# Kernel optimization log

Hardware: AMD Instinct MI355X
Metric: run time of the kernel (lower is better)

## Reference

```python
import jax, jax.numpy as jnp
import numpy as np

H = 256
N0, N1, N2 = 150000, 80000, 20000
E0, E1 = 800000, 300000


def setup_inputs() -> dict:
    key = jax.random.key(0)
    ks = jax.random.split(key, 16)
    sc = 1.0 / np.sqrt(H)
    return {
        "x": jax.random.normal(ks[0], (N0, H), jnp.float32),
        # GATConv params (heads=1): lin weight, att_src, att_dst, bias
        "W_gat": jax.random.normal(ks[1], (H, H), jnp.float32) * sc,
        "att_src": jax.random.normal(ks[2], (H,), jnp.float32) * sc,
        "att_dst": jax.random.normal(ks[3], (H,), jnp.float32) * sc,
        "b_gat": jax.random.normal(ks[4], (H,), jnp.float32) * 0.01,
        # SAGEConv layer 0: lin_l (aggregated, with bias), lin_r (root, no bias)
        "Wl0": jax.random.normal(ks[5], (H, H), jnp.float32) * sc,
        "bl0": jnp.zeros((H,), jnp.float32),
        "Wr0": jax.random.normal(ks[6], (H, H), jnp.float32) * sc,
        # SAGEConv layer 1
        "Wl1": jax.random.normal(ks[7], (H, H), jnp.float32) * sc,
        "bl1": jnp.zeros((H,), jnp.float32),
        "Wr1": jax.random.normal(ks[8], (H, H), jnp.float32) * sc,
        # NeighborSampler bipartite edge lists (src -> dst)
        "src0": jax.random.randint(ks[9], (E0,), 0, N0, dtype=jnp.int32),
        "dst0": jax.random.randint(ks[10], (E0,), 0, N1, dtype=jnp.int32),
        "src1": jax.random.randint(ks[11], (E1,), 0, N1, dtype=jnp.int32),
        "dst1": jax.random.randint(ks[12], (E1,), 0, N2, dtype=jnp.int32),
        "n1": N1,
        "n2": N2,
    }


def _gat(x, src, dst, W, a_s, a_d, b):
    """PyG GATConv, heads=1, add_self_loops=True, eval mode (dropout no-op)."""
    N = x.shape[0]
    h = x @ W                                   # [N, H]
    loops = jnp.arange(N, dtype=src.dtype)      # self loops over all N nodes
    s = jnp.concatenate([src, loops])
    d = jnp.concatenate([dst, loops])
    al_s = (h * a_s).sum(-1)                    # [N]
    al_d = (h * a_d).sum(-1)                    # [N]
    e = jax.nn.leaky_relu(al_s[s] + al_d[d], 0.2)
    m = jax.ops.segment_max(e, d, num_segments=N)     # softmax over dst groups
    w = jnp.exp(e - m[d])
    z = jax.ops.segment_sum(w, d, num_segments=N)
    coef = w / z[d]
    out = jax.ops.segment_sum(coef[:, None] * h[s], d, num_segments=N)
    return out + b


def _sage(x_src, x_tgt, src, dst, n_tgt, Wl, bl, Wr):
    """PyG SAGEConv((x, x_target), edge_index), mean aggr, normalize=True."""
    msg = x_src[src]                                         # [E, H]
    ssum = jax.ops.segment_sum(msg, dst, num_segments=n_tgt)
    cnt = jax.ops.segment_sum(jnp.ones(src.shape, msg.dtype), dst,
                              num_segments=n_tgt)
    mean = ssum / jnp.maximum(cnt, 1.0)[:, None]
    out = mean @ Wl + bl + x_tgt @ Wr
    nrm = jnp.linalg.norm(out, axis=-1, keepdims=True)       # F.normalize
    return out / jnp.maximum(nrm, 1e-12)


def reference(x, W_gat, att_src, att_dst, b_gat, Wl0, bl0, Wr0, Wl1, bl1, Wr1,
              src0, dst0, src1, dst1, n1, n2):
    # Layer 0 (its result is discarded by the original module: x = x_all each
    # iteration and only the final x is appended to xs).
    h0 = _gat(x, src0, dst0, W_gat, att_src, att_dst, b_gat)
    _ = jax.nn.relu(_sage(h0, h0[:n1], src0, dst0, n1, Wl0, bl0, Wr0))
    # Layer 1 (the returned output)
    h1 = _gat(x, src1, dst1, W_gat, att_src, att_dst, b_gat)
    out = _sage(h1, h1[:n2], src1, dst1, n2, Wl1, bl1, Wr1)
    return out
```

## Files before the change

kernel.cpp:

```cpp
#include <hip/hip_runtime.h>


#define NS 80000
#define ND 20000

typedef float   float4v  __attribute__((ext_vector_type(4)));
typedef float   f32x4    __attribute__((ext_vector_type(4)));
typedef __bf16  bf16x8   __attribute__((ext_vector_type(8)));
typedef unsigned short ushort8v __attribute__((ext_vector_type(8)));
typedef unsigned short ushort2v __attribute__((ext_vector_type(2)));
typedef int     int4v    __attribute__((ext_vector_type(4)));

union frag_u { ushort8v u; bf16x8 b; };

__device__ __forceinline__ float us2f(unsigned short u) {
    union { unsigned int i; float f; } x; x.i = ((unsigned)u) << 16; return x.f;
}
__device__ __forceinline__ unsigned short f2us(float f) {
    union { __bf16 b; unsigned short u; } x; x.b = (__bf16)f; return x.u;
}
__device__ __forceinline__ float lrelu02(float x) { return x > 0.f ? x : 0.2f * x; }

__global__ __launch_bounds__(256) void prep_misc(
    const float* __restrict__ Wg, const float* __restrict__ Wl,
    const float* __restrict__ Wr, unsigned short* __restrict__ Wgt,
    unsigned short* __restrict__ Wcat, int* __restrict__ zerop, int nz4)
{
    const int b = blockIdx.x, t = threadIdx.x;
    if (b < 256) {
        Wgt[b * 256 + t] = f2us(Wg[t * 256 + b]);
    } else if (b < 512) {
        const int n = b - 256;
        Wcat[n * 512 + t]       = f2us(Wl[t * 256 + n]);
        Wcat[n * 512 + 256 + t] = f2us(Wr[t * 256 + n]);
    } else {
        const int i = (b - 512) * 256 + t;
        if (i < nz4) ((int4v*)zerop)[i] = (int4v){0, 0, 0, 0};
    }
}

template <int EPI, bool AF32, bool COUNT>
__global__ __launch_bounds__(512) void gemm_mfma(
    const void* __restrict__ Av, const unsigned short* __restrict__ Bt,
    int M, int K,
    unsigned short* __restrict__ hb_out,
    const float* __restrict__ avs, const float* __restrict__ avd,
    float* __restrict__ al_s, float* __restrict__ al_d,
    const float* __restrict__ bias, float* __restrict__ outp,
    int nblk, const int* __restrict__ dstE, int* __restrict__ cnt,
    int* __restrict__ rank, int E)
{
    __shared__ __align__(16) unsigned short Als[2][128][40];
    __shared__ __align__(16) unsigned short Bls[2][256][40];
    __shared__ float red0[128];
    __shared__ float red1[128];

    if (COUNT && (int)blockIdx.x >= nblk) {
        const int i = ((int)blockIdx.x - nblk) * 512 + (int)threadIdx.x;
        if (i < E) rank[i] = atomicAdd(&cnt[dstE[i]], 1);
        return;
    }

    const int tid  = threadIdx.x;
    const int lane = tid & 63;
    const int wid  = tid >> 6;
    const int wr   = wid >> 2;
    const int wc   = wid & 3;
    const int row0 = blockIdx.x * 128;
    const int lg   = lane >> 4;
    const int lm   = lane & 15;

    f32x4 acc[4][4] = {};

    const int arow = tid >> 2;
    const int akof = (tid & 3) * 8;
    const int brow = tid >> 1;
    const int bkof = (tid & 1) * 16;
    const int nk   = K >> 5;

    ushort8v avr, bvr0, bvr1;

    auto load_t = [&](int kt) {
        const int k0 = kt * 32;
        if constexpr (AF32) {
            const float* ag = (const float*)Av + (size_t)(row0 + arow) * K + k0 + akof;
            const float4v v0 = *(const float4v*)ag;
            const float4v v1 = *(const float4v*)(ag + 4);
            avr[0]=f2us(v0[0]); avr[1]=f2us(v0[1]); avr[2]=f2us(v0[2]); avr[3]=f2us(v0[3]);
            avr[4]=f2us(v1[0]); avr[5]=f2us(v1[1]); avr[6]=f2us(v1[2]); avr[7]=f2us(v1[3]);
        } else {
            if (row0 + arow < M) {
                avr = *(const ushort8v*)((const unsigned short*)Av + (size_t)(row0 + arow) * K + k0 + akof);
            } else {
                avr = (ushort8v){0,0,0,0,0,0,0,0};
            }
        }
        const unsigned short* bgp = Bt + (size_t)brow * K + k0 + bkof;
        bvr0 = *(const ushort8v*)bgp;
        bvr1 = *(const ushort8v*)(bgp + 8);
    };
    auto store_t = [&](int b) {
        *(ushort8v*)&Als[b][arow][akof]     = avr;
        *(ushort8v*)&Bls[b][brow][bkof]     = bvr0;
        *(ushort8v*)&Bls[b][brow][bkof + 8] = bvr1;
    };

    load_t(0); store_t(0); __syncthreads();
    if (nk > 1) load_t(1);
    int cur = 0;

    for (int kt = 0; kt < nk; ++kt) {
        frag_u af[4], bf[4];
#pragma unroll
        for (int m = 0; m < 4; ++m)
            af[m].u = *(const ushort8v*)&Als[cur][wr*64 + m*16 + lm][lg*8];
#pragma unroll
        for (int n = 0; n < 4; ++n)
            bf[n].u = *(const ushort8v*)&Bls[cur][wc*64 + n*16 + lm][lg*8];
#pragma unroll
        for (int m = 0; m < 4; ++m)
#pragma unroll
            for (int n = 0; n < 4; ++n)
                acc[m][n] = __builtin_amdgcn_mfma_f32_16x16x32_bf16(
                    af[m].b, bf[n].b, acc[m][n], 0, 0, 0);
        if (kt + 1 < nk) {
            store_t(cur ^ 1);
            __syncthreads();
            if (kt + 2 < nk) load_t(kt + 2);
            cur ^= 1;
        }
    }

    if constexpr (EPI == 0) {
        if (tid < 128) { red0[tid] = 0.f; red1[tid] = 0.f; }
        __syncthreads();
        float asv[4], adv[4], bgv[4];
#pragma unroll
        for (int n = 0; n < 4; ++n) {
            const int col = wc*64 + n*16 + lm;
            asv[n] = avs[col]; adv[n] = avd[col]; bgv[n] = bias[col];
        }
#pragma unroll
        for (int m = 0; m < 4; ++m) {
#pragma unroll
            for (int j = 0; j < 4; ++j) {
                const int lr = wr*64 + m*16 + lg*4 + j;
                float ps = 0.f, pd = 0.f;
#pragma unroll
                for (int n = 0; n < 4; ++n) {
                    const float v = acc[m][n][j];
                    ps += v * asv[n]; pd += v * adv[n];
                    hb_out[(size_t)(row0 + lr) * 256 + wc*64 + n*16 + lm] = f2us(v + bgv[n]);
                }
#pragma unroll
                for (int off = 1; off < 16; off <<= 1) {
                    ps += __shfl_xor(ps, off);
                    pd += __shfl_xor(pd, off);
                }
                if (lm == 0) { atomicAdd(&red0[lr], ps); atomicAdd(&red1[lr], pd); }
            }
        }
        __syncthreads();
        if (tid < 128) { al_s[row0 + tid] = red0[tid]; al_d[row0 + tid] = red1[tid]; }
    } else {
        if (tid < 128) red0[tid] = 0.f;
        __syncthreads();
        float bv[4];
#pragma unroll
        for (int n = 0; n < 4; ++n) bv[n] = bias[wc*64 + n*16 + lm];
#pragma unroll
        for (int m = 0; m < 4; ++m) {
#pragma unroll
            for (int j = 0; j < 4; ++j) {
                const int lr = wr*64 + m*16 + lg*4 + j;
                float ss = 0.f;
#pragma unroll
                for (int n = 0; n < 4; ++n) {
                    const float v = acc[m][n][j] + bv[n];
                    acc[m][n][j] = v;
                    ss += v * v;
                }
#pragma unroll
                for (int off = 1; off < 16; off <<= 1) ss += __shfl_xor(ss, off);
                if (lm == 0) atomicAdd(&red0[lr], ss);
            }
        }
        __syncthreads();
#pragma unroll
        for (int m = 0; m < 4; ++m) {
#pragma unroll
            for (int j = 0; j < 4; ++j) {
                const int lr = wr*64 + m*16 + lg*4 + j;
                const int grow = row0 + lr;
                if (grow < M) {
                    const float inv = 1.0f / fmaxf(sqrtf(red0[lr]), 1e-12f);
#pragma unroll
                    for (int n = 0; n < 4; ++n)
                        outp[(size_t)grow * 256 + wc*64 + n*16 + lm] = acc[m][n][j] * inv;
                }
            }
        }
    }
}

__global__ __launch_bounds__(1024) void scan_excl(
    const int* __restrict__ cnt, int* __restrict__ ptr, int n)
{
    __shared__ int part[1024];
    const int tid = threadIdx.x;
    const int chunk = (n + 1023) / 1024;
    const int i0 = tid * chunk;
    const int i1 = min(i0 + chunk, n);
    int s = 0;
    for (int i = i0; i < i1; ++i) s += cnt[i];
    part[tid] = s;
    __syncthreads();
    for (int off = 1; off < 1024; off <<= 1) {
        const int t = (tid >= off) ? part[tid - off] : 0;
        __syncthreads();
        part[tid] += t;
        __syncthreads();
    }
    int run = tid ? part[tid - 1] : 0;
    for (int i = i0; i < i1; ++i) { ptr[i] = run; run += cnt[i]; }
    if (tid == 1023) ptr[n] = part[1023];
}

__global__ void edge_scatter(const int* __restrict__ src, const int* __restrict__ dst,
                             const int* __restrict__ ptr, const int* __restrict__ rank,
                             const float* __restrict__ al_s, const float* __restrict__ al_d,
                             int* __restrict__ ssort, float* __restrict__ wbuf, int E)
{
    const int i = blockIdx.x * 256 + threadIdx.x;
    if (i < E) {
        const int d = dst[i];
        const int s = src[i];
        const int pos = ptr[d] + rank[i];
        ssort[pos] = s;
        wbuf[pos] = __expf(lrelu02(al_s[s] + al_d[d]));
    }
}

__global__ __launch_bounds__(128) void gat_sage(
    const unsigned short* __restrict__ hb, const float* __restrict__ al_s,
    const float* __restrict__ al_d, const int* __restrict__ ssort,
    const float* __restrict__ wbuf, const int* __restrict__ ptr,
    unsigned short* __restrict__ hcat)
{
    __shared__ float ldsg[4][264];
    __shared__ float ldss[4][264];
    __shared__ float zp[4];
    const int v    = blockIdx.x;
    const int tid  = threadIdx.x;
    const int slot = tid >> 5;
    const int l32  = tid & 31;
    const int c0   = l32 * 8;
    const int p0 = ptr[v], p1 = ptr[v + 1];

    const float w_self = __expf(lrelu02(al_s[v] + al_d[v]));

    float accg[8], accs[8];
    float zpart = 0.f;
#pragma unroll
    for (int j = 0; j < 8; ++j) accs[j] = 0.f;
    if (slot == 0) {
        const ushort8v hv = *(const ushort8v*)&hb[(size_t)v * 256 + c0];
#pragma unroll
        for (int j = 0; j < 8; ++j) accg[j] = w_self * us2f(hv[j]);
    } else {
#pragma unroll
        for (int j = 0; j < 8; ++j) accg[j] = 0.f;
    }

    int p = p0 + slot;
    for (; p + 4 < p1; p += 8) {
        const int s0 = ssort[p];
        const int s1 = ssort[p + 4];
        const float w0 = wbuf[p];
        const float w1 = wbuf[p + 4];
        const ushort8v h0 = *(const ushort8v*)&hb[(size_t)s0 * 256 + c0];
        const ushort8v h1 = *(const ushort8v*)&hb[(size_t)s1 * 256 + c0];
        zpart += w0 + w1;
        const bool g0 = (s0 >= ND), g1 = (s1 >= ND);
#pragma unroll
        for (int j = 0; j < 8; ++j) {
            const float f0 = us2f(h0[j]);
            const float f1 = us2f(h1[j]);
            accg[j] = fmaf(w0, f0, accg[j]);
            accg[j] = fmaf(w1, f1, accg[j]);
            accs[j] += (g0 ? f0 : 0.f) + (g1 ? f1 : 0.f);
        }
    }
    if (p < p1) {
        const int s0 = ssort[p];
        const float w0 = wbuf[p];
        const ushort8v h0 = *(const ushort8v*)&hb[(size_t)s0 * 256 + c0];
        zpart += w0;
        const bool g0 = (s0 >= ND);
#pragma unroll
        for (int j = 0; j < 8; ++j) {
            const float f0 = us2f(h0[j]);
            accg[j] = fmaf(w0, f0, accg[j]);
            accs[j] += g0 ? f0 : 0.f;
        }
    }

    if (l32 == 0) zp[slot] = zpart;
    *(f32x4*)&ldsg[slot][c0]     = (f32x4){accg[0], accg[1], accg[2], accg[3]};
    *(f32x4*)&ldsg[slot][c0 + 4] = (f32x4){accg[4], accg[5], accg[6], accg[7]};
    *(f32x4*)&ldss[slot][c0]     = (f32x4){accs[0], accs[1], accs[2], accs[3]};
    *(f32x4*)&ldss[slot][c0 + 4] = (f32x4){accs[4], accs[5], accs[6], accs[7]};
    __syncthreads();

    const float inv_z = 1.0f / (w_self + zp[0] + zp[1] + zp[2] + zp[3]);
    const int c = tid * 2;
    float rg0 = 0.f, rg1 = 0.f, rs0 = 0.f, rs1 = 0.f;
#pragma unroll
    for (int s2 = 0; s2 < 4; ++s2) {
        rg0 += ldsg[s2][c];     rg1 += ldsg[s2][c + 1];
        rs0 += ldss[s2][c];     rs1 += ldss[s2][c + 1];
    }
    *(ushort2v*)&hcat[(size_t)v * 512 + 256 + c] =
        (ushort2v){f2us(rg0 * inv_z), f2us(rg1 * inv_z)};
    *(ushort2v*)&hcat[(size_t)v * 512 + c] =
        (ushort2v){f2us(rs0), f2us(rs1)};
}

__global__ __launch_bounds__(256) void sage_fin(
    const int* __restrict__ ssort, const int* __restrict__ ptr,
    unsigned short* __restrict__ hcat)
{
    const int tid   = threadIdx.x;
    const int g     = tid >> 6;
    const int v     = blockIdx.x * 4 + g;
    const int slot2 = (tid >> 5) & 1;
    const int l32   = tid & 31;
    const int c0    = l32 * 8;
    const int p0 = ptr[v], p1 = ptr[v + 1];

    float acc[8];
    if (slot2 == 0) {
        const ushort8v pv = *(const ushort8v*)&hcat[(size_t)v * 512 + c0];
#pragma unroll
        for (int j = 0; j < 8; ++j) acc[j] = us2f(pv[j]);
    } else {
#pragma unroll
        for (int j = 0; j < 8; ++j) acc[j] = 0.f;
    }
    int p = p0 + slot2;
    for (; p + 2 < p1; p += 4) {
        const int s0 = ssort[p];
        const int s1 = ssort[p + 2];
        if (s0 < ND) {
            const ushort8v hv = *(const ushort8v*)&hcat[(size_t)s0 * 512 + 256 + c0];
#pragma unroll
            for (int j = 0; j < 8; ++j) acc[j] += us2f(hv[j]);
        }
        if (s1 < ND) {
            const ushort8v hv = *(const ushort8v*)&hcat[(size_t)s1 * 512 + 256 + c0];
#pragma unroll
            for (int j = 0; j < 8; ++j) acc[j] += us2f(hv[j]);
        }
    }
    if (p < p1) {
        const int s0 = ssort[p];
        if (s0 < ND) {
            const ushort8v hv = *(const ushort8v*)&hcat[(size_t)s0 * 512 + 256 + c0];
#pragma unroll
            for (int j = 0; j < 8; ++j) acc[j] += us2f(hv[j]);
        }
    }
#pragma unroll
    for (int j = 0; j < 8; ++j) acc[j] += __shfl_xor(acc[j], 32);

    const int deg = p1 - p0;
    const float inv = (deg > 0) ? 1.0f / (float)deg : 0.f;
    if (slot2 == 0) {
        ushort8v o;
#pragma unroll
        for (int j = 0; j < 8; ++j) o[j] = f2us(acc[j] * inv);
        *(ushort8v*)&hcat[(size_t)v * 512 + c0] = o;
    }
}

extern "C" void kernel_launch(void* const* d_in, const int* in_sizes, int n_in,
                              void* d_out, int out_size, void* d_ws, size_t ws_size,
                              hipStream_t stream)
{
    const float* x    = (const float*)d_in[0];
    const float* Wg   = (const float*)d_in[1];
    const float* asrc = (const float*)d_in[2];
    const float* adst = (const float*)d_in[3];
    const float* bg   = (const float*)d_in[4];
    const float* Wl1  = (const float*)d_in[8];
    const float* bl1  = (const float*)d_in[9];
    const float* Wr1  = (const float*)d_in[10];
    const int*   src1 = (const int*)d_in[13];
    const int*   dst1 = (const int*)d_in[14];
    const int E1 = in_sizes[13];

    char* w = (char*)d_ws;
    unsigned short* hb   = (unsigned short*)w; w += (size_t)NS * 256 * 2;
    unsigned short* hcat = (unsigned short*)w; w += (size_t)ND * 512 * 2;
    unsigned short* Wgt  = (unsigned short*)w; w += 256 * 256 * 2;
    unsigned short* Wcat = (unsigned short*)w; w += 256 * 512 * 2;
    float* al_s = (float*)w; w += (size_t)NS * 4;
    float* al_d = (float*)w; w += (size_t)NS * 4;
    int* cnt    = (int*)w;   w += (size_t)ND * 4;
    int* ptrv   = (int*)w;   w += (size_t)(ND + 4) * 4;
    int* rank   = (int*)w;   w += (size_t)E1 * 4;
    int* ssort  = (int*)w;   w += (size_t)E1 * 4;
    float* wbuf = (float*)w; w += (size_t)E1 * 4;

    const dim3 b256(256), b512(512);
    const int nz4 = ND / 4;

    prep_misc<<<dim3(512 + (nz4 + 255) / 256), b256, 0, stream>>>(
        Wg, Wl1, Wr1, Wgt, Wcat, cnt, nz4);

    const int nblk0 = NS / 128;
    const int ncnt  = (E1 + 511) / 512;
    gemm_mfma<0, true, true><<<dim3(nblk0 + ncnt), b512, 0, stream>>>(
        x, Wgt, NS, 256, hb, asrc, adst, al_s, al_d, bg, nullptr,
        nblk0, dst1, cnt, rank, E1);

    scan_excl   <<<dim3(1), dim3(1024), 0, stream>>>(cnt, ptrv, ND);
    edge_scatter<<<dim3((E1 + 255) / 256), b256, 0, stream>>>(
        src1, dst1, ptrv, rank, al_s, al_d, ssort, wbuf, E1);

    gat_sage<<<dim3(ND), dim3(128), 0, stream>>>(hb, al_s, al_d, ssort, wbuf,
                                                 ptrv, hcat);
    sage_fin<<<dim3(ND / 4), b256, 0, stream>>>(ssort, ptrv, hcat);

    gemm_mfma<1, false, false><<<dim3((ND + 127) / 128), b512, 0, stream>>>(
        hcat, Wcat, ND, 512, nullptr, nullptr, nullptr, nullptr, nullptr,
        bl1, (float*)d_out, 0, nullptr, nullptr, nullptr, 0);
}
```

Measured before the change: 149.4 us.

## Move edge counting to separate kernel, fold scan into GEMM, bucket edges by source class

Edge counting moves out of the GEMM into a standalone count_rank kernel that keeps separate per-destination counts for sources below and above ND. The prefix scan now runs as one extra block of the first GEMM, which removes the scan_excl launch. Edge attention weights are no longer precomputed into wbuf; gat_sage recomputes them from al_s and al_d. Because edges are ordered by source class, sage_fin can loop over only the low-index sources without a per-edge branch. In exchange there is one more launch, the scan is serialized inside one 512-thread block, and each edge pays a gathered al_s read plus an exp in the aggregation kernel.

Measured after the change: 144.5 us. 1.03x faster.

```diff
diff --git a/kernel.cpp b/kernel.cpp
--- a/kernel.cpp
+++ b/kernel.cpp
@@ -39,7 +39,18 @@
     }
 }
 
-template <int EPI, bool AF32, bool COUNT>
+__global__ void count_rank(const int* __restrict__ src, const int* __restrict__ dst,
+                           int* __restrict__ cntpair, int* __restrict__ rank, int E)
+{
+    const int i = blockIdx.x * 256 + threadIdx.x;
+    if (i < E) {
+        const int d = dst[i];
+        const int cls = (src[i] < ND) ? 0 : 1;
+        rank[i] = atomicAdd(&cntpair[2 * d + cls], 1);
+    }
+}
+
+template <int EPI, bool AF32, bool SCAN>
 __global__ __launch_bounds__(512) void gemm_mfma(
     const void* __restrict__ Av, const unsigned short* __restrict__ Bt,
     int M, int K,
@@ -47,17 +58,32 @@
     const float* __restrict__ avs, const float* __restrict__ avd,
     float* __restrict__ al_s, float* __restrict__ al_d,
     const float* __restrict__ bias, float* __restrict__ outp,
-    int nblk, const int* __restrict__ dstE, int* __restrict__ cnt,
-    int* __restrict__ rank, int E)
+    int nblk, const int* __restrict__ cntpair, int* __restrict__ ptrp)
 {
     __shared__ __align__(16) unsigned short Als[2][128][40];
     __shared__ __align__(16) unsigned short Bls[2][256][40];
     __shared__ float red0[128];
     __shared__ float red1[128];
 
-    if (COUNT && (int)blockIdx.x >= nblk) {
-        const int i = ((int)blockIdx.x - nblk) * 512 + (int)threadIdx.x;
-        if (i < E) rank[i] = atomicAdd(&cnt[dstE[i]], 1);
+    if (SCAN && (int)blockIdx.x >= nblk) {
+        int* part = (int*)Als;
+        const int tid = threadIdx.x;
+        const int chunk = (ND + 511) / 512;
+        const int i0 = tid * chunk;
+        const int i1 = min(i0 + chunk, ND);
+        int s = 0;
+        for (int i = i0; i < i1; ++i) s += cntpair[2*i] + cntpair[2*i+1];
+        part[tid] = s;
+        __syncthreads();
+        for (int off = 1; off < 512; off <<= 1) {
+            const int t = (tid >= off) ? part[tid - off] : 0;
+            __syncthreads();
+            part[tid] += t;
+            __syncthreads();
+        }
+        int run = tid ? part[tid - 1] : 0;
+        for (int i = i0; i < i1; ++i) { ptrp[i] = run; run += cntpair[2*i] + cntpair[2*i+1]; }
+        if (tid == 511) ptrp[ND] = part[511];
         return;
     }
 
@@ -203,49 +229,26 @@
     }
 }
 
-__global__ __launch_bounds__(1024) void scan_excl(
-    const int* __restrict__ cnt, int* __restrict__ ptr, int n)
-{
-    __shared__ int part[1024];
-    const int tid = threadIdx.x;
-    const int chunk = (n + 1023) / 1024;
-    const int i0 = tid * chunk;
-    const int i1 = min(i0 + chunk, n);
-    int s = 0;
-    for (int i = i0; i < i1; ++i) s += cnt[i];
-    part[tid] = s;
-    __syncthreads();
-    for (int off = 1; off < 1024; off <<= 1) {
-        const int t = (tid >= off) ? part[tid - off] : 0;
-        __syncthreads();
-        part[tid] += t;
-        __syncthreads();
-    }
-    int run = tid ? part[tid - 1] : 0;
-    for (int i = i0; i < i1; ++i) { ptr[i] = run; run += cnt[i]; }
-    if (tid == 1023) ptr[n] = part[1023];
-}
-
 __global__ void edge_scatter(const int* __restrict__ src, const int* __restrict__ dst,
-                             const int* __restrict__ ptr, const int* __restrict__ rank,
-                             const float* __restrict__ al_s, const float* __restrict__ al_d,
-                             int* __restrict__ ssort, float* __restrict__ wbuf, int E)
+                             const int* __restrict__ ptrp, const int* __restrict__ rank,
+                             const int* __restrict__ cntpair,
+                             int* __restrict__ ssort, int E)
 {
     const int i = blockIdx.x * 256 + threadIdx.x;
     if (i < E) {
         const int d = dst[i];
         const int s = src[i];
-        const int pos = ptr[d] + rank[i];
+        const int base = ptrp[d];
+        const int pos = (s < ND) ? base + rank[i]
+                                 : base + cntpair[2 * d] + rank[i];
         ssort[pos] = s;
-        wbuf[pos] = __expf(lrelu02(al_s[s] + al_d[d]));
     }
 }
 
 __global__ __launch_bounds__(128) void gat_sage(
     const unsigned short* __restrict__ hb, const float* __restrict__ al_s,
     const float* __restrict__ al_d, const int* __restrict__ ssort,
-    const float* __restrict__ wbuf, const int* __restrict__ ptr,
-    unsigned short* __restrict__ hcat)
+    const int* __restrict__ ptrp, unsigned short* __restrict__ hcat)
 {
     __shared__ float ldsg[4][264];
     __shared__ float ldss[4][264];
@@ -255,9 +258,10 @@
     const int slot = tid >> 5;
     const int l32  = tid & 31;
     const int c0   = l32 * 8;
-    const int p0 = ptr[v], p1 = ptr[v + 1];
-
-    const float w_self = __expf(lrelu02(al_s[v] + al_d[v]));
+    const int p0 = ptrp[v], p1 = ptrp[v + 1];
+
+    const float ad     = al_d[v];
+    const float w_self = __expf(lrelu02(al_s[v] + ad));
 
     float accg[8], accs[8];
     float zpart = 0.f;
@@ -276,8 +280,8 @@
     for (; p + 4 < p1; p += 8) {
         const int s0 = ssort[p];
         const int s1 = ssort[p + 4];
-        const float w0 = wbuf[p];
-        const float w1 = wbuf[p + 4];
+        const float w0 = __expf(lrelu02(al_s[s0] + ad));
+        const float w1 = __expf(lrelu02(al_s[s1] + ad));
         const ushort8v h0 = *(const ushort8v*)&hb[(size_t)s0 * 256 + c0];
         const ushort8v h1 = *(const ushort8v*)&hb[(size_t)s1 * 256 + c0];
         zpart += w0 + w1;
@@ -293,7 +297,7 @@
     }
     if (p < p1) {
         const int s0 = ssort[p];
-        const float w0 = wbuf[p];
+        const float w0 = __expf(lrelu02(al_s[s0] + ad));
         const ushort8v h0 = *(const ushort8v*)&hb[(size_t)s0 * 256 + c0];
         zpart += w0;
         const bool g0 = (s0 >= ND);
@@ -327,8 +331,8 @@
 }
 
 __global__ __launch_bounds__(256) void sage_fin(
-    const int* __restrict__ ssort, const int* __restrict__ ptr,
-    unsigned short* __restrict__ hcat)
+    const int* __restrict__ ssort, const int* __restrict__ ptrp,
+    const int* __restrict__ cntpair, unsigned short* __restrict__ hcat)
 {
     const int tid   = threadIdx.x;
     const int g     = tid >> 6;
@@ -336,7 +340,9 @@
     const int slot2 = (tid >> 5) & 1;
     const int l32   = tid & 31;
     const int c0    = l32 * 8;
-    const int p0 = ptr[v], p1 = ptr[v + 1];
+    const int p0  = ptrp[v];
+    const int p1l = p0 + cntpair[2 * v];
+    const int deg = ptrp[v + 1] - p0;
 
     float acc[8];
     if (slot2 == 0) {
@@ -348,32 +354,23 @@
         for (int j = 0; j < 8; ++j) acc[j] = 0.f;
     }
     int p = p0 + slot2;
-    for (; p + 2 < p1; p += 4) {
+    for (; p + 2 < p1l; p += 4) {
         const int s0 = ssort[p];
         const int s1 = ssort[p + 2];
-        if (s0 < ND) {
-            const ushort8v hv = *(const ushort8v*)&hcat[(size_t)s0 * 512 + 256 + c0];
-#pragma unroll
-            for (int j = 0; j < 8; ++j) acc[j] += us2f(hv[j]);
-        }
-        if (s1 < ND) {
-            const ushort8v hv = *(const ushort8v*)&hcat[(size_t)s1 * 512 + 256 + c0];
-#pragma unroll
-            for (int j = 0; j < 8; ++j) acc[j] += us2f(hv[j]);
-        }
-    }
-    if (p < p1) {
+        const ushort8v h0 = *(const ushort8v*)&hcat[(size_t)s0 * 512 + 256 + c0];
+        const ushort8v h1 = *(const ushort8v*)&hcat[(size_t)s1 * 512 + 256 + c0];
+#pragma unroll
+        for (int j = 0; j < 8; ++j) acc[j] += us2f(h0[j]) + us2f(h1[j]);
+    }
+    if (p < p1l) {
         const int s0 = ssort[p];
-        if (s0 < ND) {
-            const ushort8v hv = *(const ushort8v*)&hcat[(size_t)s0 * 512 + 256 + c0];
-#pragma unroll
-            for (int j = 0; j < 8; ++j) acc[j] += us2f(hv[j]);
-        }
+        const ushort8v h0 = *(const ushort8v*)&hcat[(size_t)s0 * 512 + 256 + c0];
+#pragma unroll
+        for (int j = 0; j < 8; ++j) acc[j] += us2f(h0[j]);
     }
 #pragma unroll
     for (int j = 0; j < 8; ++j) acc[j] += __shfl_xor(acc[j], 32);
 
-    const int deg = p1 - p0;
     const float inv = (deg > 0) ? 1.0f / (float)deg : 0.f;
     if (slot2 == 0) {
         ushort8v o;
@@ -404,35 +401,35 @@
     unsigned short* hcat = (unsigned short*)w; w += (size_t)ND * 512 * 2;
     unsigned short* Wgt  = (unsigned short*)w; w += 256 * 256 * 2;
     unsigned short* Wcat = (unsigned short*)w; w += 256 * 512 * 2;
-    float* al_s = (float*)w; w += (size_t)NS * 4;
-    float* al_d = (float*)w; w += (size_t)NS * 4;
-    int* cnt    = (int*)w;   w += (size_t)ND * 4;
-    int* ptrv   = (int*)w;   w += (size_t)(ND + 4) * 4;
-    int* rank   = (int*)w;   w += (size_t)E1 * 4;
-    int* ssort  = (int*)w;   w += (size_t)E1 * 4;
-    float* wbuf = (float*)w; w += (size_t)E1 * 4;
+    float* al_s   = (float*)w; w += (size_t)NS * 4;
+    float* al_d   = (float*)w; w += (size_t)NS * 4;
+    int* cntpair  = (int*)w;   w += (size_t)2 * ND * 4;
+    int* ptrv     = (int*)w;   w += (size_t)(ND + 4) * 4;
+    int* rank     = (int*)w;   w += (size_t)E1 * 4;
+    int* ssort    = (int*)w;   w += (size_t)E1 * 4;
 
     const dim3 b256(256), b512(512);
-    const int nz4 = ND / 4;
+    const int nz4 = 2 * ND / 4;
 
     prep_misc<<<dim3(512 + (nz4 + 255) / 256), b256, 0, stream>>>(
-        Wg, Wl1, Wr1, Wgt, Wcat, cnt, nz4);
+        Wg, Wl1, Wr1, Wgt, Wcat, cntpair, nz4);
+
+    count_rank<<<dim3((E1 + 255) / 256), b256, 0, stream>>>(
+        src1, dst1, cntpair, rank, E1);
 
     const int nblk0 = NS / 128;
-    const int ncnt  = (E1 + 511) / 512;
-    gemm_mfma<0, true, true><<<dim3(nblk0 + ncnt), b512, 0, stream>>>(
+    gemm_mfma<0, true, true><<<dim3(nblk0 + 1), b512, 0, stream>>>(
         x, Wgt, NS, 256, hb, asrc, adst, al_s, al_d, bg, nullptr,
-        nblk0, dst1, cnt, rank, E1);
-
-    scan_excl   <<<dim3(1), dim3(1024), 0, stream>>>(cnt, ptrv, ND);
+        nblk0, cntpair, ptrv);
+
     edge_scatter<<<dim3((E1 + 255) / 256), b256, 0, stream>>>(
-        src1, dst1, ptrv, rank, al_s, al_d, ssort, wbuf, E1);
-
-    gat_sage<<<dim3(ND), dim3(128), 0, stream>>>(hb, al_s, al_d, ssort, wbuf,
+        src1, dst1, ptrv, rank, cntpair, ssort, E1);
+
+    gat_sage<<<dim3(ND), dim3(128), 0, stream>>>(hb, al_s, al_d, ssort,
                                                  ptrv, hcat);
-    sage_fin<<<dim3(ND / 4), b256, 0, stream>>>(ssort, ptrv, hcat);
+    sage_fin<<<dim3(ND / 4), b256, 0, stream>>>(ssort, ptrv, cntpair, hcat);
 
     gemm_mfma<1, false, false><<<dim3((ND + 127) / 128), b512, 0, stream>>>(
         hcat, Wcat, ND, 512, nullptr, nullptr, nullptr, nullptr, nullptr,
-        bl1, (float*)d_out, 0, nullptr, nullptr, nullptr, 0);
-}
+        bl1, (float*)d_out, 0, nullptr, nullptr);
+}
```
